# Kernel optimization log

Measured on AMD Instinct MI355X. Metric: run time of the kernel, lower is better.

Reference implementation:

```python
import jax, jax.numpy as jnp
import numpy as np

FORGET_BIAS = 1.0  # tf.nn.rnn_cell.LSTMCell default
HIDDEN = 64


def setup_inputs() -> dict:
    key = jax.random.key(0)
    k1, k2 = jax.random.split(key)
    B, T, D = 4096, 9, 512
    x = jax.random.normal(k1, (B, T, D), dtype=jnp.float32)
    # Fused LSTM kernel: [(D + H), 4H], gate order (i, j, f, o) as in TF LSTMCell
    kernel = jax.random.normal(k2, (D + HIDDEN, 4 * HIDDEN), dtype=jnp.float32) * 0.02
    bias = jnp.zeros((4 * HIDDEN,), dtype=jnp.float32)
    return {"x": x, "kernel": kernel, "bias": bias}


def _lstm_scan(x, kernel, bias):
    B, T, D = x.shape
    H = HIDDEN
    # Split kernel into input and recurrent parts for a cleaner scan body.
    Wx = kernel[:D]          # [D, 4H]
    Wh = kernel[D:]          # [H, 4H]
    # Precompute input contributions for all timesteps in one big GEMM.
    xg = jnp.einsum('btd,dg->btg', x, Wx) + bias  # [B, T, 4H]

    def step(carry, xg_t):
        c, h = carry
        gates = xg_t + h @ Wh  # [B, 4H]
        i, j, f, o = jnp.split(gates, 4, axis=-1)  # TF gate order: i, j, f, o
        c_new = jax.nn.sigmoid(f + FORGET_BIAS) * c + jax.nn.sigmoid(i) * jnp.tanh(j)
        h_new = jax.nn.sigmoid(o) * jnp.tanh(c_new)
        return (c_new, h_new), h_new

    c0 = jnp.zeros((B, H), dtype=x.dtype)
    h0 = jnp.zeros((B, H), dtype=x.dtype)
    _, hs = jax.lax.scan(step, (c0, h0), jnp.swapaxes(xg, 0, 1))  # hs: [T, B, H]
    return jnp.transpose(hs, (1, 0, 2))  # [B, T, H]


def reference(x, kernel, bias):
    return _lstm_scan(x, kernel, bias)
```

## Files before the change

kernel.cpp:

```cpp
#include <hip/hip_runtime.h>
#include <math.h>

#define T_STEPS 9
#define D_IN    512
#define HID     64
#define G4      256
#define BPB     8
#define ROWS    72

typedef short  short8 __attribute__((ext_vector_type(8)));
typedef float  f32x4  __attribute__((ext_vector_type(4)));
typedef unsigned int uint;
typedef unsigned short ushort;

__device__ __forceinline__ ushort f2bf(float f) {
    uint u = __float_as_uint(f);
    u = (u + 0x7FFFu + ((u >> 16) & 1u)) >> 16;
    return (ushort)u;
}
__device__ __forceinline__ float fsig(float x) {
    return 1.0f / (1.0f + __expf(-x));
}
__device__ __forceinline__ float ftanh(float x) {
    float t = __expf(-2.0f * fabsf(x));
    float r = (1.0f - t) / (1.0f + t);
    return copysignf(r, x);
}

__global__ __launch_bounds__(256)
void prep_w(const float* __restrict__ kern, ushort* __restrict__ wxT,
            ushort* __restrict__ whT)
{
    int i = blockIdx.x * 256 + threadIdx.x;
    if (i < 131072) {
        int j  = i & 7;
        int n  = (i >> 3) & 255;
        int qk = (i >> 11) & 3;
        int k0 = i >> 13;
        int k  = k0 * 32 + qk * 8 + j;
        wxT[i] = f2bf(kern[(size_t)k * G4 + n]);
    } else {
        int i2 = i - 131072;
        int j  = i2 & 7;
        int n  = (i2 >> 3) & 255;
        int kq = i2 >> 11;
        whT[i2] = f2bf(kern[(size_t)(D_IN + kq * 8 + j) * G4 + n]);
    }
}

__global__ __launch_bounds__(256, 2)
void lstm_fused(const float* __restrict__ x, const ushort* __restrict__ wxT,
                const ushort* __restrict__ whT, const float* __restrict__ bias,
                float* __restrict__ out)
{
    __shared__ ushort sAm[80 * 512];
    ushort* const sH = &sAm[72 * 512];

    const int t = threadIdx.x;
    const int w = t >> 6, l = t & 63;
    const int lane15 = l & 15, quad = l >> 4;
    const int u = w * 16 + lane15;

    {
        uint4 z = {0u, 0u, 0u, 0u};
        ((uint4*)&sAm[72 * 512])[t]       = z;
        ((uint4*)&sAm[72 * 512])[t + 256] = z;
    }

    short8 bFb[2][4];
    {
        const ushort* wxc = wxT + (size_t)(0 * 4 + quad) * 256 * 8;
        #pragma unroll
        for (int g = 0; g < 4; ++g)
            bFb[0][g] = *(const short8*)&wxc[(size_t)(g * 64 + u) * 8];
    }

    const float4* xblk = (const float4*)(x + (size_t)blockIdx.x * (ROWS * D_IN));
    #pragma unroll
    for (int h = 0; h < 2; ++h) {
        float4 v[18];
        #pragma unroll
        for (int q = 0; q < 18; ++q)
            v[q] = xblk[(h * 18 + q) * 256 + t];
        #pragma unroll
        for (int q = 0; q < 18; ++q) {
            int flat = (h * 18 + q) * 256 + t;
            int r    = flat >> 7;
            int colq = flat & 127;
            int b = r / 9, s = r - b * 9;
            int row = s * 8 + b;
            int kq  = colq >> 1;
            int adr = row * 512 + ((kq ^ (row & 7)) << 3) + ((colq & 1) << 2);
            uint2 p;
            p.x = f2bf(v[q].x) | ((uint)f2bf(v[q].y) << 16);
            p.y = f2bf(v[q].z) | ((uint)f2bf(v[q].w) << 16);
            *(uint2*)&sAm[adr] = p;
        }
    }
    __syncthreads();

    f32x4 acc[5][4];
    #pragma unroll
    for (int i = 0; i < 5; ++i)
        #pragma unroll
        for (int g = 0; g < 4; ++g)
            acc[i][g] = (f32x4){0.f, 0.f, 0.f, 0.f};

    #pragma unroll
    for (int k = 0; k < 16; ++k) {
        if (k < 15) {
            const ushort* wxc = wxT + (size_t)((k + 1) * 4 + quad) * 256 * 8;
            #pragma unroll
            for (int g = 0; g < 4; ++g)
                bFb[(k + 1) & 1][g] = *(const short8*)&wxc[(size_t)(g * 64 + u) * 8];
        }
        #pragma unroll
        for (int i = 0; i < 5; ++i) {
            int row = i * 16 + lane15;
            short8 aF = *(const short8*)
                &sAm[row * 512 + (((k * 4 + quad) ^ (row & 7)) << 3)];
            #pragma unroll
            for (int g = 0; g < 4; ++g)
                acc[i][g] = __builtin_amdgcn_mfma_f32_16x16x32_bf16(aF, bFb[k & 1][g], acc[i][g], 0, 0, 0);
        }
    }

    short8 whF[4][2];
    #pragma unroll
    for (int g = 0; g < 4; ++g)
        #pragma unroll
        for (int kh = 0; kh < 2; ++kh)
            whF[g][kh] = *(const short8*)&whT[(size_t)((kh * 4 + quad) * 256 + g * 64 + u) * 8];

    float bia[4];
    bia[0] = bias[u];
    bia[1] = bias[64 + u];
    bia[2] = bias[128 + u] + 1.0f;
    bia[3] = bias[192 + u];

    float cst[4] = {0.f, 0.f, 0.f, 0.f};
    const int b0 = blockIdx.x * BPB;

    #pragma unroll
    for (int s = 0; s < T_STEPS; ++s) {
        const int  i = s >> 1;
        const int  p = s & 1;
        const bool active = ((quad >> 1) == p);
        const int  bofs = (quad & 1) * 4;

        f32x4 g4[4];
        #pragma unroll
        for (int g = 0; g < 4; ++g)
            #pragma unroll
            for (int r = 0; r < 4; ++r)
                g4[g][r] = acc[i][g][r] + bia[g];

        short8 aF[2];
        #pragma unroll
        for (int kh = 0; kh < 2; ++kh)
            aF[kh] = *(const short8*)&sH[((kh * 4 + quad) * 16 + lane15) * 8];

        #pragma unroll
        for (int g = 0; g < 4; ++g)
            #pragma unroll
            for (int kh = 0; kh < 2; ++kh)
                g4[g] = __builtin_amdgcn_mfma_f32_16x16x32_bf16(aF[kh], whF[g][kh], g4[g], 0, 0, 0);

        __syncthreads();

        const int wrow = 8 * ((s + 1) & 1);
        #pragma unroll
        for (int r = 0; r < 4; ++r) {
            float cp = __shfl_xor(cst[r], 32);
            if (active) {
                float ii = fsig(g4[0][r]);
                float jj = ftanh(g4[1][r]);
                float ff = fsig(g4[2][r]);
                float oo = fsig(g4[3][r]);
                float c  = ff * cp + ii * jj;
                cst[r] = c;
                float h = oo * ftanh(c);
                int bb = bofs + r;
                out[((size_t)(b0 + bb) * T_STEPS + s) * HID + u] = h;
                sH[((u >> 3) * 16 + wrow + bb) * 8 + (u & 7)] = f2bf(h);
            }
        }
        __syncthreads();
    }
}

extern "C" void kernel_launch(void* const* d_in, const int* in_sizes, int n_in,
                              void* d_out, int out_size, void* d_ws, size_t ws_size,
                              hipStream_t stream)
{
    const float* x    = (const float*)d_in[0];
    const float* kern = (const float*)d_in[1];
    const float* bias = (const float*)d_in[2];
    float* out = (float*)d_out;

    const int B = in_sizes[0] / (T_STEPS * D_IN);

    ushort* wxT = (ushort*)d_ws;
    ushort* whT = (ushort*)((char*)d_ws + 262144);

    prep_w<<<576, 256, 0, stream>>>(kern, wxT, whT);
    lstm_fused<<<B / BPB, 256, 0, stream>>>(x, wxT, whT, bias, out);
}
```

Measured before the change: 127.1 us.

## Stream x into LDS in triple-buffered chunks via direct global-to-LDS loads

The input tile is no longer loaded whole through registers and converted to bf16 before any MFMA runs. It is now fetched in 64-column chunks with global_load_lds into a triple-buffered fp32 LDS ring, with explicit vmcnt waits so loading overlaps the input GEMM. Conversion to bf16 moves to the operand-load side using v_cvt_pk_bf16_f32. The weight prep kernel is rewritten to emit vector stores from fewer blocks, and one barrier in the recurrent loop is removed. This risks a race on sH, since the read-before-write barrier is gone. It also uses more LDS (about 60KB per block), which may limit occupancy to two blocks.

```diff
diff --git a/kernel.cpp b/kernel.cpp
--- a/kernel.cpp
+++ b/kernel.cpp
@@ -7,6 +7,7 @@
 #define G4      256
 #define BPB     8
 #define ROWS    72
+#define NCH     8
 
 typedef short  short8 __attribute__((ext_vector_type(8)));
 typedef float  f32x4  __attribute__((ext_vector_type(4)));
@@ -26,26 +27,33 @@
     float r = (1.0f - t) / (1.0f + t);
     return copysignf(r, x);
 }
+__device__ __forceinline__ short8 cvt8(f32x4 lo, f32x4 hi) {
+    union { uint u[4]; short8 s; } r;
+    asm("v_cvt_pk_bf16_f32 %0, %1, %2" : "=v"(r.u[0]) : "v"(lo[0]), "v"(lo[1]));
+    asm("v_cvt_pk_bf16_f32 %0, %1, %2" : "=v"(r.u[1]) : "v"(lo[2]), "v"(lo[3]));
+    asm("v_cvt_pk_bf16_f32 %0, %1, %2" : "=v"(r.u[2]) : "v"(hi[0]), "v"(hi[1]));
+    asm("v_cvt_pk_bf16_f32 %0, %1, %2" : "=v"(r.u[3]) : "v"(hi[2]), "v"(hi[3]));
+    return r.s;
+}
+__device__ __forceinline__ void gl2lds16(const float* g, float* l) {
+    __builtin_amdgcn_global_load_lds(
+        (const __attribute__((address_space(1))) void*)g,
+        (__attribute__((address_space(3))) void*)l, 16, 0, 0);
+}
 
 __global__ __launch_bounds__(256)
 void prep_w(const float* __restrict__ kern, ushort* __restrict__ wxT,
             ushort* __restrict__ whT)
 {
-    int i = blockIdx.x * 256 + threadIdx.x;
-    if (i < 131072) {
-        int j  = i & 7;
-        int n  = (i >> 3) & 255;
-        int qk = (i >> 11) & 3;
-        int k0 = i >> 13;
-        int k  = k0 * 32 + qk * 8 + j;
-        wxT[i] = f2bf(kern[(size_t)k * G4 + n]);
-    } else {
-        int i2 = i - 131072;
-        int j  = i2 & 7;
-        int n  = (i2 >> 3) & 255;
-        int kq = i2 >> 11;
-        whT[i2] = f2bf(kern[(size_t)(D_IN + kq * 8 + j) * G4 + n]);
-    }
+    const int blk = blockIdx.x;
+    const int n   = threadIdx.x;
+    const int krow0 = (blk < 64) ? blk * 8 : 512 + (blk - 64) * 8;
+    union { ushort us[8]; short8 v; } o;
+    #pragma unroll
+    for (int j = 0; j < 8; ++j)
+        o.us[j] = f2bf(kern[(size_t)(krow0 + j) * G4 + n]);
+    if (blk < 64) *(short8*)&wxT[((size_t)blk * 256 + n) * 8] = o.v;
+    else          *(short8*)&whT[((size_t)(blk - 64) * 256 + n) * 8] = o.v;
 }
 
 __global__ __launch_bounds__(256, 2)
@@ -53,51 +61,40 @@
                 const ushort* __restrict__ whT, const float* __restrict__ bias,
                 float* __restrict__ out)
 {
-    __shared__ ushort sAm[80 * 512];
-    ushort* const sH = &sAm[72 * 512];
+    __shared__ float  sX[3][80 * 64];
+    __shared__ ushort sH[1024];
 
     const int t = threadIdx.x;
     const int w = t >> 6, l = t & 63;
     const int lane15 = l & 15, quad = l >> 4;
     const int u = w * 16 + lane15;
 
-    {
+    const float* xbase = x + (size_t)blockIdx.x * (ROWS * D_IN);
+    int soff[5];
+    #pragma unroll
+    for (int j = 0; j < 5; ++j) {
+        int m   = w * 5 + j;
+        int row = m * 4 + (l >> 4);
+        int b_  = row & 7, s_ = row >> 3;
+        int xr  = b_ * 9 + (s_ < 9 ? s_ : 8);
+        int oct = ((l & 15) >> 1) ^ (row & 7);
+        soff[j] = xr * 512 + oct * 8 + (l & 1) * 4;
+    }
+
+    #pragma unroll
+    for (int j = 0; j < 5; ++j)
+        gl2lds16(xbase + soff[j] + 0 * 64, &sX[0][(w * 5 + j) * 256]);
+    __builtin_amdgcn_sched_barrier(0);
+    #pragma unroll
+    for (int j = 0; j < 5; ++j)
+        gl2lds16(xbase + soff[j] + 1 * 64, &sX[1][(w * 5 + j) * 256]);
+    __builtin_amdgcn_sched_barrier(0);
+
+    if (t < 128) {
         uint4 z = {0u, 0u, 0u, 0u};
-        ((uint4*)&sAm[72 * 512])[t]       = z;
-        ((uint4*)&sAm[72 * 512])[t + 256] = z;
-    }
-
-    short8 bFb[2][4];
-    {
-        const ushort* wxc = wxT + (size_t)(0 * 4 + quad) * 256 * 8;
-        #pragma unroll
-        for (int g = 0; g < 4; ++g)
-            bFb[0][g] = *(const short8*)&wxc[(size_t)(g * 64 + u) * 8];
-    }
-
-    const float4* xblk = (const float4*)(x + (size_t)blockIdx.x * (ROWS * D_IN));
-    #pragma unroll
-    for (int h = 0; h < 2; ++h) {
-        float4 v[18];
-        #pragma unroll
-        for (int q = 0; q < 18; ++q)
-            v[q] = xblk[(h * 18 + q) * 256 + t];
-        #pragma unroll
-        for (int q = 0; q < 18; ++q) {
-            int flat = (h * 18 + q) * 256 + t;
-            int r    = flat >> 7;
-            int colq = flat & 127;
-            int b = r / 9, s = r - b * 9;
-            int row = s * 8 + b;
-            int kq  = colq >> 1;
-            int adr = row * 512 + ((kq ^ (row & 7)) << 3) + ((colq & 1) << 2);
-            uint2 p;
-            p.x = f2bf(v[q].x) | ((uint)f2bf(v[q].y) << 16);
-            p.y = f2bf(v[q].z) | ((uint)f2bf(v[q].w) << 16);
-            *(uint2*)&sAm[adr] = p;
-        }
-    }
-    __syncthreads();
+        *(uint4*)&sH[t * 8] = z;
+    }
+    asm volatile("s_waitcnt lgkmcnt(0)" ::: "memory");
 
     f32x4 acc[5][4];
     #pragma unroll
@@ -106,22 +103,46 @@
         for (int g = 0; g < 4; ++g)
             acc[i][g] = (f32x4){0.f, 0.f, 0.f, 0.f};
 
-    #pragma unroll
-    for (int k = 0; k < 16; ++k) {
-        if (k < 15) {
-            const ushort* wxc = wxT + (size_t)((k + 1) * 4 + quad) * 256 * 8;
+    short8 bFb[2][4];
+
+    #pragma unroll
+    for (int k = 0; k < NCH; ++k) {
+        if (k < NCH - 1) asm volatile("s_waitcnt vmcnt(5)" ::: "memory");
+        else             asm volatile("s_waitcnt vmcnt(0)" ::: "memory");
+        __builtin_amdgcn_sched_barrier(0);
+        __builtin_amdgcn_s_barrier();
+        __builtin_amdgcn_sched_barrier(0);
+
+        #pragma unroll
+        for (int kk = 0; kk < 2; ++kk)
             #pragma unroll
             for (int g = 0; g < 4; ++g)
-                bFb[(k + 1) & 1][g] = *(const short8*)&wxc[(size_t)(g * 64 + u) * 8];
+                bFb[kk][g] = *(const short8*)
+                    &wxT[(size_t)(((k * 2 + kk) * 4 + quad) * 256 + g * 64 + u) * 8];
+        __builtin_amdgcn_sched_barrier(0);
+
+        if (k < NCH - 2) {
+            float* dst = &sX[(k + 2) % 3][0];
+            #pragma unroll
+            for (int j = 0; j < 5; ++j)
+                gl2lds16(xbase + soff[j] + (k + 2) * 64, dst + (w * 5 + j) * 256);
         }
-        #pragma unroll
-        for (int i = 0; i < 5; ++i) {
-            int row = i * 16 + lane15;
-            short8 aF = *(const short8*)
-                &sAm[row * 512 + (((k * 4 + quad) ^ (row & 7)) << 3)];
-            #pragma unroll
-            for (int g = 0; g < 4; ++g)
-                acc[i][g] = __builtin_amdgcn_mfma_f32_16x16x32_bf16(aF, bFb[k & 1][g], acc[i][g], 0, 0, 0);
+        __builtin_amdgcn_sched_barrier(0);
+
+        #pragma unroll
+        for (int kk = 0; kk < 2; ++kk) {
+            #pragma unroll
+            for (int i = 0; i < 5; ++i) {
+                int row = i * 16 + lane15;
+                int op  = (((kk * 4 + quad) ^ (row & 7)) << 3);
+                f32x4 lo = *(const f32x4*)&sX[k % 3][row * 64 + op];
+                f32x4 hi = *(const f32x4*)&sX[k % 3][row * 64 + op + 4];
+                short8 aF = cvt8(lo, hi);
+                #pragma unroll
+                for (int g = 0; g < 4; ++g)
+                    acc[i][g] = __builtin_amdgcn_mfma_f32_16x16x32_bf16(
+                        aF, bFb[kk][g], acc[i][g], 0, 0, 0);
+            }
         }
     }
 
@@ -165,8 +186,6 @@
             #pragma unroll
             for (int kh = 0; kh < 2; ++kh)
                 g4[g] = __builtin_amdgcn_mfma_f32_16x16x32_bf16(aF[kh], whF[g][kh], g4[g], 0, 0, 0);
-
-        __syncthreads();
 
         const int wrow = 8 * ((s + 1) & 1);
         #pragma unroll
@@ -185,7 +204,10 @@
                 sH[((u >> 3) * 16 + wrow + bb) * 8 + (u & 7)] = f2bf(h);
             }
         }
-        __syncthreads();
+        asm volatile("s_waitcnt lgkmcnt(0)" ::: "memory");
+        __builtin_amdgcn_sched_barrier(0);
+        __builtin_amdgcn_s_barrier();
+        __builtin_amdgcn_sched_barrier(0);
     }
 }
 
@@ -203,6 +225,6 @@
     ushort* wxT = (ushort*)d_ws;
     ushort* whT = (ushort*)((char*)d_ws + 262144);
 
-    prep_w<<<576, 256, 0, stream>>>(kern, wxT, whT);
+    prep_w<<<72, 256, 0, stream>>>(kern, wxT, whT);
     lstm_fused<<<B / BPB, 256, 0, stream>>>(x, wxT, whT, bias, out);
 }
```

New measurement: 125.1 us. About the same (-1.5%).
